# Performance work log

Hardware: AMD Instinct MI355X
Metric: run time of the kernel (lower is better)

The kernel has to match this reference:

```python
import jax, jax.numpy as jnp
import numpy as np

NUM_CLASSES = 10000
EMBED = 512
BATCH = 4096
EPS = 1e-12
MAXV = 1e12


def cosine_distance(x, y):
    # 1 - cosine similarity, computed via normalized matmul
    xn = x / jnp.linalg.norm(x, axis=1, keepdims=True)
    yn = y / jnp.linalg.norm(y, axis=1, keepdims=True)
    return 1.0 - jnp.einsum('bd,cd->bc', xn, yn)


def setup_inputs() -> dict:
    key = jax.random.key(0)
    k1, k2, k3 = jax.random.split(key, 3)
    features = jax.random.normal(k1, (BATCH, EMBED), dtype=jnp.float32)
    centers = jax.random.normal(k2, (NUM_CLASSES, EMBED), dtype=jnp.float32)
    targets = jax.random.randint(k3, (BATCH,), 0, NUM_CLASSES, dtype=jnp.int32)
    return {"features": features, "centers": centers, "targets": targets}


def reference(features, centers, targets):
    batch_size = features.shape[0]
    distmat = cosine_distance(features, centers)          # (B, C)
    classes = jnp.arange(NUM_CLASSES, dtype=targets.dtype)
    mask = (targets[:, None] == classes[None, :]).astype(distmat.dtype)  # (B, C)
    dist = distmat * mask
    loss = jnp.clip(dist, EPS, MAXV).sum() / batch_size
    return loss
```

## Files before the change

kernel.cpp:

```cpp
#include <hip/hip_runtime.h>
#include <math.h>


#define BATCH_N 4096
#define EMBED_N 512
#define NUM_CLASSES_N 10000
#define EPS_F 1e-12f
#define MAXV_F 1e12f

__global__ __launch_bounds__(256) void center_loss_rows(
    const float* __restrict__ features,
    const float* __restrict__ centers,
    const int*   __restrict__ targets,
    float*       __restrict__ row_out)
{
    const int wave = threadIdx.x >> 6;
    const int lane = threadIdx.x & 63;
    const int b = blockIdx.x * 4 + wave;
    if (b >= BATCH_N) return;

    const int t = targets[b];
    const float4* f4 = (const float4*)(features + (size_t)b * EMBED_N);
    const float4* c4 = (const float4*)(centers  + (size_t)t * EMBED_N);

    float dot = 0.f, ff = 0.f, cc = 0.f;
    #pragma unroll
    for (int k = 0; k < 2; ++k) {
        const float4 fv = f4[lane + 64 * k];
        const float4 cv = c4[lane + 64 * k];
        dot += fv.x * cv.x + fv.y * cv.y + fv.z * cv.z + fv.w * cv.w;
        ff  += fv.x * fv.x + fv.y * fv.y + fv.z * fv.z + fv.w * fv.w;
        cc  += cv.x * cv.x + cv.y * cv.y + cv.z * cv.z + cv.w * cv.w;
    }

    #pragma unroll
    for (int off = 32; off >= 1; off >>= 1) {
        dot += __shfl_xor(dot, off, 64);
        ff  += __shfl_xor(ff,  off, 64);
        cc  += __shfl_xor(cc,  off, 64);
    }

    if (lane == 0) {
        float d = 1.0f - dot / (sqrtf(ff) * sqrtf(cc));
        d = fminf(fmaxf(d, EPS_F), MAXV_F);
        row_out[b] = d;
    }
}

__global__ __launch_bounds__(256) void center_loss_reduce(
    const float* __restrict__ row_vals,
    float*       __restrict__ out)
{
    __shared__ float sdata[4];
    const int tid = threadIdx.x;

    float s = 0.f;
    #pragma unroll
    for (int k = 0; k < BATCH_N / 256; ++k) s += row_vals[tid + 256 * k];

    #pragma unroll
    for (int off = 32; off >= 1; off >>= 1) s += __shfl_xor(s, off, 64);

    if ((tid & 63) == 0) sdata[tid >> 6] = s;
    __syncthreads();
    if (tid == 0) {
        const float tot = sdata[0] + sdata[1] + sdata[2] + sdata[3];
        out[0] = tot * (1.0f / BATCH_N)
               + (float)((double)(NUM_CLASSES_N - 1) * 1e-12);
    }
}

extern "C" void kernel_launch(void* const* d_in, const int* in_sizes, int n_in,
                              void* d_out, int out_size, void* d_ws, size_t ws_size,
                              hipStream_t stream) {
    const float* features = (const float*)d_in[0];
    const float* centers  = (const float*)d_in[1];
    const int*   targets  = (const int*)d_in[2];
    float* out = (float*)d_out;
    float* row_vals = (float*)d_ws;

    center_loss_rows<<<BATCH_N / 4, 256, 0, stream>>>(features, centers, targets, row_vals);
    center_loss_reduce<<<1, 256, 0, stream>>>(row_vals, out);
}
```

Before: 11.78 us.

## Fuse row and reduce kernels via fixed-point atomics and last-block ticket

Merges the per-row cosine-distance kernel and the single-block reduction into one kernel. Each block sums its four row values, converts the sum to a 64-bit fixed-point integer and atomically adds it to a global accumulator. A ticket counter lets the last block write the final scaled loss. This removes the second kernel launch and the round trip through the row-value buffer, but adds a memset of the workspace before the launch, global atomics, and fixed-point quantization of the per-block sums.

```diff
diff --git a/kernel.cpp b/kernel.cpp
--- a/kernel.cpp
+++ b/kernel.cpp
@@ -8,16 +8,20 @@
 #define EPS_F 1e-12f
 #define MAXV_F 1e12f
 
-__global__ __launch_bounds__(256) void center_loss_rows(
+#define FP_SCALE 17592186044416.0
+#define INV_FP_SCALE (1.0 / 17592186044416.0)
+
+__global__ __launch_bounds__(256) void center_loss_fused(
     const float* __restrict__ features,
     const float* __restrict__ centers,
     const int*   __restrict__ targets,
-    float*       __restrict__ row_out)
+    unsigned long long* __restrict__ acc,
+    unsigned*    __restrict__ ticket,
+    float*       __restrict__ out)
 {
     const int wave = threadIdx.x >> 6;
     const int lane = threadIdx.x & 63;
     const int b = blockIdx.x * 4 + wave;
-    if (b >= BATCH_N) return;
 
     const int t = targets[b];
     const float4* f4 = (const float4*)(features + (size_t)b * EMBED_N);
@@ -40,33 +44,26 @@
         cc  += __shfl_xor(cc,  off, 64);
     }
 
+    __shared__ float sd[4];
     if (lane == 0) {
         float d = 1.0f - dot / (sqrtf(ff) * sqrtf(cc));
-        d = fminf(fmaxf(d, EPS_F), MAXV_F);
-        row_out[b] = d;
+        sd[wave] = fminf(fmaxf(d, EPS_F), MAXV_F);
     }
-}
+    __syncthreads();
 
-__global__ __launch_bounds__(256) void center_loss_reduce(
-    const float* __restrict__ row_vals,
-    float*       __restrict__ out)
-{
-    __shared__ float sdata[4];
-    const int tid = threadIdx.x;
-
-    float s = 0.f;
-    #pragma unroll
-    for (int k = 0; k < BATCH_N / 256; ++k) s += row_vals[tid + 256 * k];
-
-    #pragma unroll
-    for (int off = 32; off >= 1; off >>= 1) s += __shfl_xor(s, off, 64);
-
-    if ((tid & 63) == 0) sdata[tid >> 6] = s;
-    __syncthreads();
-    if (tid == 0) {
-        const float tot = sdata[0] + sdata[1] + sdata[2] + sdata[3];
-        out[0] = tot * (1.0f / BATCH_N)
-               + (float)((double)(NUM_CLASSES_N - 1) * 1e-12);
+    if (threadIdx.x == 0) {
+        const float bs = sd[0] + sd[1] + sd[2] + sd[3];
+        const unsigned long long q =
+            (unsigned long long)((double)bs * FP_SCALE);
+        atomicAdd(acc, q);
+        __threadfence();
+        const unsigned old = atomicAdd(ticket, 1u);
+        if (old == gridDim.x - 1) {
+            __threadfence();
+            const unsigned long long tot = atomicAdd(acc, 0ull);
+            out[0] = (float)((double)tot * INV_FP_SCALE * (1.0 / BATCH_N)
+                             + (double)(NUM_CLASSES_N - 1) * 1e-12);
+        }
     }
 }
 
@@ -77,8 +74,11 @@
     const float* centers  = (const float*)d_in[1];
     const int*   targets  = (const int*)d_in[2];
     float* out = (float*)d_out;
-    float* row_vals = (float*)d_ws;
 
-    center_loss_rows<<<BATCH_N / 4, 256, 0, stream>>>(features, centers, targets, row_vals);
-    center_loss_reduce<<<1, 256, 0, stream>>>(row_vals, out);
+    unsigned long long* acc = (unsigned long long*)d_ws;
+    unsigned* ticket = (unsigned*)((char*)d_ws + 8);
+
+    hipMemsetAsync(d_ws, 0, 16, stream);
+    center_loss_fused<<<BATCH_N / 4, 256, 0, stream>>>(
+        features, centers, targets, acc, ticket, out);
 }
```

Result: slower. 36.62 us (+210.9%).
